# Optimization experiments

Measured on AMD Instinct MI355X. Metric: run time of the kernel, lower is better.

## Reference

```python
import jax, jax.numpy as jnp
import numpy as np


def setup_inputs() -> dict:
    key = jax.random.key(0)
    k1, k2 = jax.random.split(key, 2)
    x = jax.random.normal(k1, (16, 64, 256, 256), dtype=jnp.float32)
    w_off = jax.random.normal(k2, (2, 64), dtype=jnp.float32) * 0.05  # 1x1 conv kernel [out=2, in=ch]
    b_off = jnp.zeros((2,), dtype=jnp.float32)
    return {"x": x, "w_off": w_off, "b_off": b_off}


def _bilinear_grid_sample(x, gx, gy):
    """grid_sample(x, grid, align_corners=False, padding_mode='zeros').
    x: [B,C,H,W]; gx,gy: [B,H,W] normalized coords in [-1,1] (+offset)."""
    B, C, H, W = x.shape
    # unnormalize (align_corners=False): pix = ((g+1)*size - 1)/2
    px = ((gx + 1.0) * W - 1.0) * 0.5
    py = ((gy + 1.0) * H - 1.0) * 0.5
    x0f = jnp.floor(px)
    y0f = jnp.floor(py)
    wx1 = px - x0f  # frac weights
    wy1 = py - y0f
    x0 = x0f.astype(jnp.int32)
    y0 = y0f.astype(jnp.int32)

    def corner(xi, yi):
        valid = (xi >= 0) & (xi < W) & (yi >= 0) & (yi < H)
        xc = jnp.clip(xi, 0, W - 1)
        yc = jnp.clip(yi, 0, H - 1)
        # per-batch gather: img[:, yb, xb] -> [C,H,W]
        v = jax.vmap(lambda img, yb, xb: img[:, yb, xb])(x, yc, xc)  # [B,C,H,W]
        return v * valid[:, None, :, :].astype(x.dtype)

    v00 = corner(x0, y0)
    v01 = corner(x0 + 1, y0)
    v10 = corner(x0, y0 + 1)
    v11 = corner(x0 + 1, y0 + 1)
    wx1e = wx1[:, None, :, :]
    wy1e = wy1[:, None, :, :]
    return (v00 * (1.0 - wx1e) * (1.0 - wy1e)
            + v01 * wx1e * (1.0 - wy1e)
            + v10 * (1.0 - wx1e) * wy1e
            + v11 * wx1e * wy1e)


def reference(x, w_off, b_off):
    B, C, H, W = x.shape
    # 1x1 conv (ch -> 2) + tanh, scaled by 0.5
    offset = jnp.tanh(jnp.einsum('bchw,oc->bohw', x, w_off)
                      + b_off[None, :, None, None]) * 0.5  # [B,2,H,W]
    yy = jnp.linspace(-1.0, 1.0, H, dtype=x.dtype)
    xx = jnp.linspace(-1.0, 1.0, W, dtype=x.dtype)
    gy_base, gx_base = jnp.meshgrid(yy, xx, indexing='ij')  # [H,W]
    # grid = stack([xx, yy], -1) + offset.permute(0,2,3,1): channel0 -> x, channel1 -> y
    gx = gx_base[None] + offset[:, 0]
    gy = gy_base[None] + offset[:, 1]
    return _bilinear_grid_sample(x, gx, gy)
```

## Files before the change

### kernel.cpp

```cpp
#include <hip/hip_runtime.h>

#define BB 16
#define CC 64
#define HH 256
#define WW 256
#define HW (HH * WW)

#define XT_BYTES 134217728ULL
#define NEED_WS  (XT_BYTES + 8388608ULL)

typedef float    fx4 __attribute__((ext_vector_type(4)));
typedef unsigned ux4 __attribute__((ext_vector_type(4)));

__device__ __forceinline__ unsigned f2bf(float f) {
    unsigned u = __float_as_uint(f);
    u += 0x7FFFu + ((u >> 16) & 1u);
    return u >> 16;
}
__device__ __forceinline__ float bflo(unsigned w) { return __uint_as_float(w << 16); }
__device__ __forceinline__ float bfhi(unsigned w) { return __uint_as_float(w & 0xFFFF0000u); }

__global__ __launch_bounds__(256) void k_prep(
    const float* __restrict__ x, const float* __restrict__ w_off, const float* __restrict__ b_off,
    unsigned* __restrict__ xt, float2* __restrict__ pq)
{
    __shared__ unsigned s_pack[CC / 2][WW + 1];
    __shared__ float sw0[CC], sw1[CC];
    const int t = threadIdx.x;
    if (t < CC)          sw0[t]      = w_off[t];
    else if (t < 2 * CC) sw1[t - CC] = w_off[t];
    __syncthreads();
    const int row = blockIdx.x & (HH - 1);
    const int b   = blockIdx.x >> 8;
    const float* __restrict__ xb = x + (size_t)b * CC * HW + row * WW + t;
    float a0 = 0.f, a1 = 0.f, vprev = 0.f;
#pragma unroll 16
    for (int c = 0; c < CC; ++c) {
        const float v = xb[(size_t)c * HW];
        a0 = fmaf(v, sw0[c], a0);
        a1 = fmaf(v, sw1[c], a1);
        if (c & 1) s_pack[c >> 1][t] = f2bf(vprev) | (f2bf(v) << 16);
        vprev = v;
    }
    const float offx = tanhf(a0 + b_off[0]) * 0.5f;
    const float offy = tanhf(a1 + b_off[1]) * 0.5f;
    const float gx = -1.0f + (float)t   * (2.0f / (WW - 1)) + offx;
    const float gy = -1.0f + (float)row * (2.0f / (HH - 1)) + offy;
    pq[(size_t)b * HW + row * WW + t] =
        make_float2(((gx + 1.0f) * (float)WW - 1.0f) * 0.5f, ((gy + 1.0f) * (float)HH - 1.0f) * 0.5f);
    __syncthreads();
    const int j  = t & 7;
    const int pb = t >> 3;
    unsigned* __restrict__ xto = xt + ((size_t)b * HW + (size_t)row * WW) * 32;
#pragma unroll
    for (int g = 0; g < 8; ++g) {
        const int p = g * 32 + pb;
        ux4 v;
        v.x = s_pack[4 * j + 0][p];
        v.y = s_pack[4 * j + 1][p];
        v.z = s_pack[4 * j + 2][p];
        v.w = s_pack[4 * j + 3][p];
        __builtin_nontemporal_store(v, reinterpret_cast<ux4*>(xto + (size_t)p * 32 + j * 4));
    }
}

__global__ __launch_bounds__(256) void k_sample4(
    const unsigned* __restrict__ xt, const float2* __restrict__ pq, float* __restrict__ out)
{
    const int raw = blockIdx.x;
    const int lb  = (raw & 7) * 1024 + (raw >> 3);
    const int half = lb & 1;
    const int row  = (lb >> 1) & (HH - 1);
    const int b    = lb >> 9;

    __shared__ float so[2][CC][65];

    const int t  = threadIdx.x;
    const int l8 = t & 7;
    const int ps = t >> 3;
    const int px0 = half * 128;

    const unsigned* __restrict__ xb = xt + (size_t)b * HW * 32;
    const float2* __restrict__ pqr = pq + (size_t)b * HW + row * WW + px0;

    const float2 prA0 = pqr[ps];
    const float2 prB0 = pqr[32 + ps];
    const float2 prA1 = pqr[64 + ps];
    const float2 prB1 = pqr[96 + ps];

#define COORDS(prc, W00, W01, W10, W11, I00, I01, I10, I11)                         \
    {                                                                               \
        const float x0f = floorf(prc.x), y0f = floorf(prc.y);                       \
        const float wx1 = prc.x - x0f,  wy1 = prc.y - y0f;                          \
        const float wx0 = 1.f - wx1,   wy0 = 1.f - wy1;                             \
        const int x0 = (int)x0f, y0 = (int)y0f, x1 = x0 + 1, y1 = y0 + 1;           \
        const bool vx0 = (unsigned)x0 < WW, vx1 = (unsigned)x1 < WW;                \
        const bool vy0 = (unsigned)y0 < HH, vy1 = (unsigned)y1 < HH;                \
        const int cx0 = min(max(x0, 0), WW - 1), cx1 = min(max(x1, 0), WW - 1);     \
        const int cy0 = min(max(y0, 0), HH - 1), cy1 = min(max(y1, 0), HH - 1);     \
        W00 = (vx0 && vy0) ? wx0 * wy0 : 0.f;                                       \
        W01 = (vx1 && vy0) ? wx1 * wy0 : 0.f;                                       \
        W10 = (vx0 && vy1) ? wx0 * wy1 : 0.f;                                       \
        W11 = (vx1 && vy1) ? wx1 * wy1 : 0.f;                                       \
        I00 = (unsigned)(cy0 * WW + cx0) * 32u + l8 * 4u;                           \
        I01 = (unsigned)(cy0 * WW + cx1) * 32u + l8 * 4u;                           \
        I10 = (unsigned)(cy1 * WW + cx0) * 32u + l8 * 4u;                           \
        I11 = (unsigned)(cy1 * WW + cx1) * 32u + l8 * 4u;                           \
    }

    float wA00, wA01, wA10, wA11, wB00, wB01, wB10, wB11;
    float uA00, uA01, uA10, uA11, uB00, uB01, uB10, uB11;
    unsigned iA00, iA01, iA10, iA11, iB00, iB01, iB10, iB11;
    unsigned jA00, jA01, jA10, jA11, jB00, jB01, jB10, jB11;
    COORDS(prA0, wA00, wA01, wA10, wA11, iA00, iA01, iA10, iA11)
    COORDS(prB0, wB00, wB01, wB10, wB11, iB00, iB01, iB10, iB11)
    COORDS(prA1, uA00, uA01, uA10, uA11, jA00, jA01, jA10, jA11)
    COORDS(prB1, uB00, uB01, uB10, uB11, jB00, jB01, jB10, jB11)

    const uint4 vA00 = *reinterpret_cast<const uint4*>(xb + iA00);
    const uint4 vA01 = *reinterpret_cast<const uint4*>(xb + iA01);
    const uint4 vA10 = *reinterpret_cast<const uint4*>(xb + iA10);
    const uint4 vA11 = *reinterpret_cast<const uint4*>(xb + iA11);
    const uint4 vB00 = *reinterpret_cast<const uint4*>(xb + iB00);
    const uint4 vB01 = *reinterpret_cast<const uint4*>(xb + iB01);
    const uint4 vB10 = *reinterpret_cast<const uint4*>(xb + iB10);
    const uint4 vB11 = *reinterpret_cast<const uint4*>(xb + iB11);
    const uint4 yA00 = *reinterpret_cast<const uint4*>(xb + jA00);
    const uint4 yA01 = *reinterpret_cast<const uint4*>(xb + jA01);
    const uint4 yA10 = *reinterpret_cast<const uint4*>(xb + jA10);
    const uint4 yA11 = *reinterpret_cast<const uint4*>(xb + jA11);
    const uint4 yB00 = *reinterpret_cast<const uint4*>(xb + jB00);
    const uint4 yB01 = *reinterpret_cast<const uint4*>(xb + jB01);
    const uint4 yB10 = *reinterpret_cast<const uint4*>(xb + jB10);
    const uint4 yB11 = *reinterpret_cast<const uint4*>(xb + jB11);

    const int c8 = l8 * 8;

#define BLEND_STORE(BUF, V00, V01, V10, V11, W00, W01, W10, W11, PXL)               \
    {                                                                               \
        float f0 = W00 * bflo(V00.x); float f1 = W00 * bfhi(V00.x);                 \
        float f2 = W00 * bflo(V00.y); float f3 = W00 * bfhi(V00.y);                 \
        float f4 = W00 * bflo(V00.z); float f5 = W00 * bfhi(V00.z);                 \
        float f6 = W00 * bflo(V00.w); float f7 = W00 * bfhi(V00.w);                 \
        f0 = fmaf(W01, bflo(V01.x), f0); f1 = fmaf(W01, bfhi(V01.x), f1);           \
        f2 = fmaf(W01, bflo(V01.y), f2); f3 = fmaf(W01, bfhi(V01.y), f3);           \
        f4 = fmaf(W01, bflo(V01.z), f4); f5 = fmaf(W01, bfhi(V01.z), f5);           \
        f6 = fmaf(W01, bflo(V01.w), f6); f7 = fmaf(W01, bfhi(V01.w), f7);           \
        f0 = fmaf(W10, bflo(V10.x), f0); f1 = fmaf(W10, bfhi(V10.x), f1);           \
        f2 = fmaf(W10, bflo(V10.y), f2); f3 = fmaf(W10, bfhi(V10.y), f3);           \
        f4 = fmaf(W10, bflo(V10.z), f4); f5 = fmaf(W10, bfhi(V10.z), f5);           \
        f6 = fmaf(W10, bflo(V10.w), f6); f7 = fmaf(W10, bfhi(V10.w), f7);           \
        f0 = fmaf(W11, bflo(V11.x), f0); f1 = fmaf(W11, bfhi(V11.x), f1);           \
        f2 = fmaf(W11, bflo(V11.y), f2); f3 = fmaf(W11, bfhi(V11.y), f3);           \
        f4 = fmaf(W11, bflo(V11.z), f4); f5 = fmaf(W11, bfhi(V11.z), f5);           \
        f6 = fmaf(W11, bflo(V11.w), f6); f7 = fmaf(W11, bfhi(V11.w), f7);           \
        so[BUF][c8 + 0][PXL] = f0; so[BUF][c8 + 1][PXL] = f1;                       \
        so[BUF][c8 + 2][PXL] = f2; so[BUF][c8 + 3][PXL] = f3;                       \
        so[BUF][c8 + 4][PXL] = f4; so[BUF][c8 + 5][PXL] = f5;                       \
        so[BUF][c8 + 6][PXL] = f6; so[BUF][c8 + 7][PXL] = f7;                       \
    }

#define WRITEOUT(BUF, QOFF)                                                         \
    {                                                                               \
        const int p  = t & 15;                                                      \
        const int cg = (t >> 4) & 3;                                                \
        const int wv = t >> 6;                                                      \
        float* __restrict__ ob = out + (size_t)b * CC * HW + row * WW + px0 + QOFF; \
        _Pragma("unroll")                                                           \
        for (int it = 0; it < 4; ++it) {                                            \
            const int c = wv * 16 + it * 4 + cg;                                    \
            fx4 r;                                                                  \
            r.x = so[BUF][c][4 * p + 0];                                            \
            r.y = so[BUF][c][4 * p + 1];                                            \
            r.z = so[BUF][c][4 * p + 2];                                            \
            r.w = so[BUF][c][4 * p + 3];                                            \
            __builtin_nontemporal_store(r, reinterpret_cast<fx4*>(ob + (size_t)c * HW + 4 * p)); \
        }                                                                           \
    }

    BLEND_STORE(0, vA00, vA01, vA10, vA11, wA00, wA01, wA10, wA11, ps)
    BLEND_STORE(0, vB00, vB01, vB10, vB11, wB00, wB01, wB10, wB11, (32 + ps))
    __syncthreads();
    WRITEOUT(0, 0)
    BLEND_STORE(1, yA00, yA01, yA10, yA11, uA00, uA01, uA10, uA11, ps)
    BLEND_STORE(1, yB00, yB01, yB10, yB11, uB00, uB01, uB10, uB11, (32 + ps))
    __syncthreads();
    WRITEOUT(1, 64)
}

__global__ __launch_bounds__(256) void k_offsets(
    const float* __restrict__ x, const float* __restrict__ w_off, const float* __restrict__ b_off,
    float2* __restrict__ pq)
{
    __shared__ float s_w0[CC];
    __shared__ float s_w1[CC];
    if (threadIdx.x < CC)          s_w0[threadIdx.x]      = w_off[threadIdx.x];
    else if (threadIdx.x < 2 * CC) s_w1[threadIdx.x - CC] = w_off[threadIdx.x];
    __syncthreads();
    const int t    = blockIdx.x * blockDim.x + threadIdx.x;
    const int pix0 = t * 4;
    const int w = pix0 & (WW - 1);
    const int h = (pix0 >> 8) & (HH - 1);
    const int b = pix0 >> 16;
    const float* __restrict__ xb = x + (size_t)b * CC * HW + h * WW + w;
    float a0[4] = {0.f, 0.f, 0.f, 0.f};
    float a1[4] = {0.f, 0.f, 0.f, 0.f};
#pragma unroll 8
    for (int c = 0; c < CC; ++c) {
        const float4 v = *reinterpret_cast<const float4*>(xb + (size_t)c * HW);
        const float w0 = s_w0[c], w1 = s_w1[c];
        a0[0] = fmaf(v.x, w0, a0[0]); a1[0] = fmaf(v.x, w1, a1[0]);
        a0[1] = fmaf(v.y, w0, a0[1]); a1[1] = fmaf(v.y, w1, a1[1]);
        a0[2] = fmaf(v.z, w0, a0[2]); a1[2] = fmaf(v.z, w1, a1[2]);
        a0[3] = fmaf(v.w, w0, a0[3]); a1[3] = fmaf(v.w, w1, a1[3]);
    }
    const float b0 = b_off[0], b1 = b_off[1];
#pragma unroll
    for (int j = 0; j < 4; ++j) {
        const float offx = tanhf(a0[j] + b0) * 0.5f;
        const float offy = tanhf(a1[j] + b1) * 0.5f;
        const float gx = -1.0f + (float)(w + j) * (2.0f / (WW - 1)) + offx;
        const float gy = -1.0f + (float)h       * (2.0f / (HH - 1)) + offy;
        pq[pix0 + j] = make_float2(((gx + 1.0f) * (float)WW - 1.0f) * 0.5f,
                                   ((gy + 1.0f) * (float)HH - 1.0f) * 0.5f);
    }
}

__global__ __launch_bounds__(256, 4) void k_sample(
    const float* __restrict__ x, const float2* __restrict__ pq, float* __restrict__ out)
{
    const int bid = blockIdx.x;
    const int c = bid & (CC - 1);
    const int b = bid >> 6;
    const float* __restrict__ xp = x   + ((size_t)b * CC + c) * HW;
    float* __restrict__       op = out + ((size_t)b * CC + c) * HW;
    const float2* __restrict__ pqb = pq + (size_t)b * HW;
    const int w = threadIdx.x;
    for (int k0 = 0; k0 < HH; k0 += 4) {
        int   i00[4], i01[4], i10[4], i11[4];
        float w00[4], w01[4], w10[4], w11[4];
#pragma unroll
        for (int j = 0; j < 4; ++j) {
            const float2 p = pqb[(k0 + j) * WW + w];
            const float x0f = floorf(p.x);
            const float y0f = floorf(p.y);
            const float wx1 = p.x - x0f;
            const float wy1 = p.y - y0f;
            const float wx0 = 1.0f - wx1;
            const float wy0 = 1.0f - wy1;
            const int x0 = (int)x0f, y0 = (int)y0f;
            const int x1 = x0 + 1,   y1 = y0 + 1;
            const bool vx0 = (unsigned)x0 < WW;
            const bool vx1 = (unsigned)x1 < WW;
            const bool vy0 = (unsigned)y0 < HH;
            const bool vy1 = (unsigned)y1 < HH;
            const int cx0 = min(max(x0, 0), WW - 1);
            const int cx1 = min(max(x1, 0), WW - 1);
            const int cy0 = min(max(y0, 0), HH - 1);
            const int cy1 = min(max(y1, 0), HH - 1);
            w00[j] = (vx0 && vy0) ? wx0 * wy0 : 0.f;
            w01[j] = (vx1 && vy0) ? wx1 * wy0 : 0.f;
            w10[j] = (vx0 && vy1) ? wx0 * wy1 : 0.f;
            w11[j] = (vx1 && vy1) ? wx1 * wy1 : 0.f;
            i00[j] = cy0 * WW + cx0;
            i01[j] = cy0 * WW + cx1;
            i10[j] = cy1 * WW + cx0;
            i11[j] = cy1 * WW + cx1;
        }
        float v00[4], v01[4], v10[4], v11[4];
#pragma unroll
        for (int j = 0; j < 4; ++j) v00[j] = xp[i00[j]];
#pragma unroll
        for (int j = 0; j < 4; ++j) v01[j] = xp[i01[j]];
#pragma unroll
        for (int j = 0; j < 4; ++j) v10[j] = xp[i10[j]];
#pragma unroll
        for (int j = 0; j < 4; ++j) v11[j] = xp[i11[j]];
#pragma unroll
        for (int j = 0; j < 4; ++j) {
            float v = w00[j] * v00[j];
            v = fmaf(w01[j], v01[j], v);
            v = fmaf(w10[j], v10[j], v);
            v = fmaf(w11[j], v11[j], v);
            __builtin_nontemporal_store(v, &op[(k0 + j) * WW + w]);
        }
    }
}

extern "C" void kernel_launch(void* const* d_in, const int* in_sizes, int n_in,
                              void* d_out, int out_size, void* d_ws, size_t ws_size,
                              hipStream_t stream) {
    const float* x     = (const float*)d_in[0];
    const float* w_off = (const float*)d_in[1];
    const float* b_off = (const float*)d_in[2];
    float* out = (float*)d_out;

    if (ws_size >= NEED_WS) {
        unsigned* xt = (unsigned*)d_ws;
        float2*   pq = (float2*)((char*)d_ws + XT_BYTES);
        k_prep<<<BB * HH, 256, 0, stream>>>(x, w_off, b_off, xt, pq);
        k_sample4<<<BB * HH * 2, 256, 0, stream>>>(xt, pq, out);
    } else {
        float2* pq = (float2*)d_ws;
        const int grid1 = (BB * HW / 4) / 256;
        k_offsets<<<grid1, 256, 0, stream>>>(x, w_off, b_off, pq);
        k_sample<<<BB * CC, 256, 0, stream>>>(x, pq, out);
    }
}
```

Baseline: 189.1 us.

## Software-pipeline prep and sampling across batch groups with mixed-role kernels

Splits the batch into groups of four and launches mixed kernels whose blocks either transpose/pack the next group or sample the previous group, interleaved at a 1:2 ratio. The aim is to overlap the read-heavy prep phase with the gather/write-heavy sampling phase so both HBM directions and compute stay busy, and to shrink the bf16 working set touched at once so it stays more cache-resident. In exchange it adds launches, a shared-memory union sized to the larger role (possibly lowering occupancy), and block-role divergence.

```diff
diff --git a/kernel.cpp b/kernel.cpp
--- a/kernel.cpp
+++ b/kernel.cpp
@@ -9,6 +9,10 @@
 #define XT_BYTES 134217728ULL
 #define NEED_WS  (XT_BYTES + 8388608ULL)
 
+#define NBG   4
+#define PBLK  (NBG * HH)
+#define SBLK  (NBG * HH * 2)
+
 typedef float    fx4 __attribute__((ext_vector_type(4)));
 typedef unsigned ux4 __attribute__((ext_vector_type(4)));
 
@@ -20,73 +24,43 @@
 __device__ __forceinline__ float bflo(unsigned w) { return __uint_as_float(w << 16); }
 __device__ __forceinline__ float bfhi(unsigned w) { return __uint_as_float(w & 0xFFFF0000u); }
 
-__global__ __launch_bounds__(256) void k_prep(
-    const float* __restrict__ x, const float* __restrict__ w_off, const float* __restrict__ b_off,
-    unsigned* __restrict__ xt, float2* __restrict__ pq)
-{
-    __shared__ unsigned s_pack[CC / 2][WW + 1];
-    __shared__ float sw0[CC], sw1[CC];
-    const int t = threadIdx.x;
-    if (t < CC)          sw0[t]      = w_off[t];
-    else if (t < 2 * CC) sw1[t - CC] = w_off[t];
-    __syncthreads();
-    const int row = blockIdx.x & (HH - 1);
-    const int b   = blockIdx.x >> 8;
-    const float* __restrict__ xb = x + (size_t)b * CC * HW + row * WW + t;
-    float a0 = 0.f, a1 = 0.f, vprev = 0.f;
-#pragma unroll 16
-    for (int c = 0; c < CC; ++c) {
-        const float v = xb[(size_t)c * HW];
-        a0 = fmaf(v, sw0[c], a0);
-        a1 = fmaf(v, sw1[c], a1);
-        if (c & 1) s_pack[c >> 1][t] = f2bf(vprev) | (f2bf(v) << 16);
-        vprev = v;
-    }
-    const float offx = tanhf(a0 + b_off[0]) * 0.5f;
-    const float offy = tanhf(a1 + b_off[1]) * 0.5f;
-    const float gx = -1.0f + (float)t   * (2.0f / (WW - 1)) + offx;
-    const float gy = -1.0f + (float)row * (2.0f / (HH - 1)) + offy;
-    pq[(size_t)b * HW + row * WW + t] =
-        make_float2(((gx + 1.0f) * (float)WW - 1.0f) * 0.5f, ((gy + 1.0f) * (float)HH - 1.0f) * 0.5f);
-    __syncthreads();
-    const int j  = t & 7;
-    const int pb = t >> 3;
-    unsigned* __restrict__ xto = xt + ((size_t)b * HW + (size_t)row * WW) * 32;
-#pragma unroll
-    for (int g = 0; g < 8; ++g) {
-        const int p = g * 32 + pb;
-        ux4 v;
-        v.x = s_pack[4 * j + 0][p];
-        v.y = s_pack[4 * j + 1][p];
-        v.z = s_pack[4 * j + 2][p];
-        v.w = s_pack[4 * j + 3][p];
-        __builtin_nontemporal_store(v, reinterpret_cast<ux4*>(xto + (size_t)p * 32 + j * 4));
-    }
-}
-
-__global__ __launch_bounds__(256) void k_sample4(
-    const unsigned* __restrict__ xt, const float2* __restrict__ pq, float* __restrict__ out)
-{
-    const int raw = blockIdx.x;
-    const int lb  = (raw & 7) * 1024 + (raw >> 3);
-    const int half = lb & 1;
-    const int row  = (lb >> 1) & (HH - 1);
-    const int b    = lb >> 9;
-
-    __shared__ float so[2][CC][65];
-
-    const int t  = threadIdx.x;
-    const int l8 = t & 7;
-    const int ps = t >> 3;
-    const int px0 = half * 128;
-
-    const unsigned* __restrict__ xb = xt + (size_t)b * HW * 32;
-    const float2* __restrict__ pqr = pq + (size_t)b * HW + row * WW + px0;
-
-    const float2 prA0 = pqr[ps];
-    const float2 prB0 = pqr[32 + ps];
-    const float2 prA1 = pqr[64 + ps];
-    const float2 prB1 = pqr[96 + ps];
+#define PREP_BODY(B_, ROW_, PACK_, W0_, W1_)                                        \
+    {                                                                               \
+        if (t < CC)          W0_[t]      = w_off[t];                                \
+        else if (t < 2*CC)   W1_[t - CC] = w_off[t];                                \
+        __syncthreads();                                                            \
+        const float* __restrict__ xb = x + (size_t)(B_) * CC * HW + (ROW_) * WW + t;\
+        float a0 = 0.f, a1 = 0.f, vprev = 0.f;                                      \
+        _Pragma("unroll 16")                                                        \
+        for (int c = 0; c < CC; ++c) {                                              \
+            const float v = xb[(size_t)c * HW];                                     \
+            a0 = fmaf(v, W0_[c], a0);                                               \
+            a1 = fmaf(v, W1_[c], a1);                                               \
+            if (c & 1) PACK_[c >> 1][t] = f2bf(vprev) | (f2bf(v) << 16);            \
+            vprev = v;                                                              \
+        }                                                                           \
+        const float offx = tanhf(a0 + b_off[0]) * 0.5f;                             \
+        const float offy = tanhf(a1 + b_off[1]) * 0.5f;                             \
+        const float gx = -1.0f + (float)t      * (2.0f / (WW - 1)) + offx;          \
+        const float gy = -1.0f + (float)(ROW_) * (2.0f / (HH - 1)) + offy;          \
+        pq[(size_t)(B_) * HW + (ROW_) * WW + t] =                                   \
+            make_float2(((gx + 1.0f) * (float)WW - 1.0f) * 0.5f,                    \
+                        ((gy + 1.0f) * (float)HH - 1.0f) * 0.5f);                   \
+        __syncthreads();                                                            \
+        const int j  = t & 7;                                                       \
+        const int pb = t >> 3;                                                      \
+        unsigned* __restrict__ xto = xt + ((size_t)(B_) * HW + (size_t)(ROW_) * WW) * 32; \
+        _Pragma("unroll")                                                           \
+        for (int g = 0; g < 8; ++g) {                                               \
+            const int p = g * 32 + pb;                                              \
+            ux4 v;                                                                  \
+            v.x = PACK_[4 * j + 0][p];                                              \
+            v.y = PACK_[4 * j + 1][p];                                              \
+            v.z = PACK_[4 * j + 2][p];                                              \
+            v.w = PACK_[4 * j + 3][p];                                              \
+            __builtin_nontemporal_store(v, reinterpret_cast<ux4*>(xto + (size_t)p * 32 + j * 4)); \
+        }                                                                           \
+    }
 
 #define COORDS(prc, W00, W01, W10, W11, I00, I01, I10, I11)                         \
     {                                                                               \
@@ -108,35 +82,7 @@
         I11 = (unsigned)(cy1 * WW + cx1) * 32u + l8 * 4u;                           \
     }
 
-    float wA00, wA01, wA10, wA11, wB00, wB01, wB10, wB11;
-    float uA00, uA01, uA10, uA11, uB00, uB01, uB10, uB11;
-    unsigned iA00, iA01, iA10, iA11, iB00, iB01, iB10, iB11;
-    unsigned jA00, jA01, jA10, jA11, jB00, jB01, jB10, jB11;
-    COORDS(prA0, wA00, wA01, wA10, wA11, iA00, iA01, iA10, iA11)
-    COORDS(prB0, wB00, wB01, wB10, wB11, iB00, iB01, iB10, iB11)
-    COORDS(prA1, uA00, uA01, uA10, uA11, jA00, jA01, jA10, jA11)
-    COORDS(prB1, uB00, uB01, uB10, uB11, jB00, jB01, jB10, jB11)
-
-    const uint4 vA00 = *reinterpret_cast<const uint4*>(xb + iA00);
-    const uint4 vA01 = *reinterpret_cast<const uint4*>(xb + iA01);
-    const uint4 vA10 = *reinterpret_cast<const uint4*>(xb + iA10);
-    const uint4 vA11 = *reinterpret_cast<const uint4*>(xb + iA11);
-    const uint4 vB00 = *reinterpret_cast<const uint4*>(xb + iB00);
-    const uint4 vB01 = *reinterpret_cast<const uint4*>(xb + iB01);
-    const uint4 vB10 = *reinterpret_cast<const uint4*>(xb + iB10);
-    const uint4 vB11 = *reinterpret_cast<const uint4*>(xb + iB11);
-    const uint4 yA00 = *reinterpret_cast<const uint4*>(xb + jA00);
-    const uint4 yA01 = *reinterpret_cast<const uint4*>(xb + jA01);
-    const uint4 yA10 = *reinterpret_cast<const uint4*>(xb + jA10);
-    const uint4 yA11 = *reinterpret_cast<const uint4*>(xb + jA11);
-    const uint4 yB00 = *reinterpret_cast<const uint4*>(xb + jB00);
-    const uint4 yB01 = *reinterpret_cast<const uint4*>(xb + jB01);
-    const uint4 yB10 = *reinterpret_cast<const uint4*>(xb + jB10);
-    const uint4 yB11 = *reinterpret_cast<const uint4*>(xb + jB11);
-
-    const int c8 = l8 * 8;
-
-#define BLEND_STORE(BUF, V00, V01, V10, V11, W00, W01, W10, W11, PXL)               \
+#define BLEND_STORE(SO_, BUF, V00, V01, V10, V11, W00, W01, W10, W11, PXL)          \
     {                                                                               \
         float f0 = W00 * bflo(V00.x); float f1 = W00 * bfhi(V00.x);                 \
         float f2 = W00 * bflo(V00.y); float f3 = W00 * bfhi(V00.y);                 \
@@ -154,38 +100,127 @@
         f2 = fmaf(W11, bflo(V11.y), f2); f3 = fmaf(W11, bfhi(V11.y), f3);           \
         f4 = fmaf(W11, bflo(V11.z), f4); f5 = fmaf(W11, bfhi(V11.z), f5);           \
         f6 = fmaf(W11, bflo(V11.w), f6); f7 = fmaf(W11, bfhi(V11.w), f7);           \
-        so[BUF][c8 + 0][PXL] = f0; so[BUF][c8 + 1][PXL] = f1;                       \
-        so[BUF][c8 + 2][PXL] = f2; so[BUF][c8 + 3][PXL] = f3;                       \
-        so[BUF][c8 + 4][PXL] = f4; so[BUF][c8 + 5][PXL] = f5;                       \
-        so[BUF][c8 + 6][PXL] = f6; so[BUF][c8 + 7][PXL] = f7;                       \
-    }
-
-#define WRITEOUT(BUF, QOFF)                                                         \
+        SO_[BUF][c8 + 0][PXL] = f0; SO_[BUF][c8 + 1][PXL] = f1;                     \
+        SO_[BUF][c8 + 2][PXL] = f2; SO_[BUF][c8 + 3][PXL] = f3;                     \
+        SO_[BUF][c8 + 4][PXL] = f4; SO_[BUF][c8 + 5][PXL] = f5;                     \
+        SO_[BUF][c8 + 6][PXL] = f6; SO_[BUF][c8 + 7][PXL] = f7;                     \
+    }
+
+#define WRITEOUT(SO_, BUF, B_, ROW_, PX0_, QOFF)                                    \
     {                                                                               \
         const int p  = t & 15;                                                      \
         const int cg = (t >> 4) & 3;                                                \
         const int wv = t >> 6;                                                      \
-        float* __restrict__ ob = out + (size_t)b * CC * HW + row * WW + px0 + QOFF; \
+        float* __restrict__ ob = out + (size_t)(B_) * CC * HW + (ROW_) * WW + (PX0_) + QOFF; \
         _Pragma("unroll")                                                           \
         for (int it = 0; it < 4; ++it) {                                            \
             const int c = wv * 16 + it * 4 + cg;                                    \
             fx4 r;                                                                  \
-            r.x = so[BUF][c][4 * p + 0];                                            \
-            r.y = so[BUF][c][4 * p + 1];                                            \
-            r.z = so[BUF][c][4 * p + 2];                                            \
-            r.w = so[BUF][c][4 * p + 3];                                            \
+            r.x = SO_[BUF][c][4 * p + 0];                                           \
+            r.y = SO_[BUF][c][4 * p + 1];                                           \
+            r.z = SO_[BUF][c][4 * p + 2];                                           \
+            r.w = SO_[BUF][c][4 * p + 3];                                           \
             __builtin_nontemporal_store(r, reinterpret_cast<fx4*>(ob + (size_t)c * HW + 4 * p)); \
         }                                                                           \
     }
 
-    BLEND_STORE(0, vA00, vA01, vA10, vA11, wA00, wA01, wA10, wA11, ps)
-    BLEND_STORE(0, vB00, vB01, vB10, vB11, wB00, wB01, wB10, wB11, (32 + ps))
-    __syncthreads();
-    WRITEOUT(0, 0)
-    BLEND_STORE(1, yA00, yA01, yA10, yA11, uA00, uA01, uA10, uA11, ps)
-    BLEND_STORE(1, yB00, yB01, yB10, yB11, uB00, uB01, uB10, uB11, (32 + ps))
-    __syncthreads();
-    WRITEOUT(1, 64)
+#define SAMPLE_BODY(B_, ROW_, HALF_, SO_)                                           \
+    {                                                                               \
+        const int l8 = t & 7;                                                       \
+        const int ps = t >> 3;                                                      \
+        const int px0 = (HALF_) * 128;                                              \
+        const unsigned* __restrict__ xb = xt + (size_t)(B_) * HW * 32;              \
+        const float2* __restrict__ pqr = pq + (size_t)(B_) * HW + (ROW_) * WW + px0;\
+        const float2 prA0 = pqr[ps];                                                \
+        const float2 prB0 = pqr[32 + ps];                                           \
+        const float2 prA1 = pqr[64 + ps];                                           \
+        const float2 prB1 = pqr[96 + ps];                                           \
+        float wA00, wA01, wA10, wA11, wB00, wB01, wB10, wB11;                       \
+        float uA00, uA01, uA10, uA11, uB00, uB01, uB10, uB11;                       \
+        unsigned iA00, iA01, iA10, iA11, iB00, iB01, iB10, iB11;                    \
+        unsigned jA00, jA01, jA10, jA11, jB00, jB01, jB10, jB11;                    \
+        COORDS(prA0, wA00, wA01, wA10, wA11, iA00, iA01, iA10, iA11)                \
+        COORDS(prB0, wB00, wB01, wB10, wB11, iB00, iB01, iB10, iB11)                \
+        COORDS(prA1, uA00, uA01, uA10, uA11, jA00, jA01, jA10, jA11)                \
+        COORDS(prB1, uB00, uB01, uB10, uB11, jB00, jB01, jB10, jB11)                \
+        const uint4 vA00 = *reinterpret_cast<const uint4*>(xb + iA00);              \
+        const uint4 vA01 = *reinterpret_cast<const uint4*>(xb + iA01);              \
+        const uint4 vA10 = *reinterpret_cast<const uint4*>(xb + iA10);              \
+        const uint4 vA11 = *reinterpret_cast<const uint4*>(xb + iA11);              \
+        const uint4 vB00 = *reinterpret_cast<const uint4*>(xb + iB00);              \
+        const uint4 vB01 = *reinterpret_cast<const uint4*>(xb + iB01);              \
+        const uint4 vB10 = *reinterpret_cast<const uint4*>(xb + iB10);              \
+        const uint4 vB11 = *reinterpret_cast<const uint4*>(xb + iB11);              \
+        const uint4 yA00 = *reinterpret_cast<const uint4*>(xb + jA00);              \
+        const uint4 yA01 = *reinterpret_cast<const uint4*>(xb + jA01);              \
+        const uint4 yA10 = *reinterpret_cast<const uint4*>(xb + jA10);              \
+        const uint4 yA11 = *reinterpret_cast<const uint4*>(xb + jA11);              \
+        const uint4 yB00 = *reinterpret_cast<const uint4*>(xb + jB00);              \
+        const uint4 yB01 = *reinterpret_cast<const uint4*>(xb + jB01);              \
+        const uint4 yB10 = *reinterpret_cast<const uint4*>(xb + jB10);              \
+        const uint4 yB11 = *reinterpret_cast<const uint4*>(xb + jB11);              \
+        const int c8 = l8 * 8;                                                      \
+        BLEND_STORE(SO_, 0, vA00, vA01, vA10, vA11, wA00, wA01, wA10, wA11, ps)     \
+        BLEND_STORE(SO_, 0, vB00, vB01, vB10, vB11, wB00, wB01, wB10, wB11, (32 + ps)) \
+        __syncthreads();                                                            \
+        WRITEOUT(SO_, 0, B_, ROW_, px0, 0)                                          \
+        BLEND_STORE(SO_, 1, yA00, yA01, yA10, yA11, uA00, uA01, uA10, uA11, ps)     \
+        BLEND_STORE(SO_, 1, yB00, yB01, yB10, yB11, uB00, uB01, uB10, uB11, (32 + ps)) \
+        __syncthreads();                                                            \
+        WRITEOUT(SO_, 1, B_, ROW_, px0, 64)                                         \
+    }
+
+__global__ __launch_bounds__(256) void k_prep(
+    const float* __restrict__ x, const float* __restrict__ w_off, const float* __restrict__ b_off,
+    unsigned* __restrict__ xt, float2* __restrict__ pq, int pbase)
+{
+    __shared__ unsigned s_pack[CC / 2][WW + 1];
+    __shared__ float sw0[CC], sw1[CC];
+    const int t   = threadIdx.x;
+    const int bid = blockIdx.x;
+    const int b   = pbase + (bid >> 8);
+    const int row = bid & 255;
+    PREP_BODY(b, row, s_pack, sw0, sw1)
+}
+
+__global__ __launch_bounds__(256) void k_sample4(
+    const unsigned* __restrict__ xt, const float2* __restrict__ pq, float* __restrict__ out,
+    int sbase)
+{
+    __shared__ float so[2][CC][65];
+    const int t   = threadIdx.x;
+    const int raw = blockIdx.x;
+    const int lb  = (raw & 7) * (SBLK / 8) + (raw >> 3);
+    const int half = lb & 1;
+    const int row  = (lb >> 1) & (HH - 1);
+    const int b    = sbase + (lb >> 9);
+    SAMPLE_BODY(b, row, half, so)
+}
+
+union MixSh {
+    struct { unsigned pack[CC / 2][WW + 1]; float w0[CC], w1[CC]; } p;
+    float so[2][CC][65];
+};
+__global__ __launch_bounds__(256) void k_mix(
+    const float* __restrict__ x, const float* __restrict__ w_off, const float* __restrict__ b_off,
+    unsigned* __restrict__ xt, float2* __restrict__ pq, float* __restrict__ out,
+    int pbase, int sbase)
+{
+    __shared__ MixSh sh;
+    const int t   = threadIdx.x;
+    const int bid = blockIdx.x;
+    if (bid % 3 == 0) {
+        const int pidx = bid / 3;
+        const int b    = pbase + (pidx >> 8);
+        const int row  = pidx & 255;
+        PREP_BODY(b, row, sh.p.pack, sh.p.w0, sh.p.w1)
+    } else {
+        const int sidx = (bid / 3) * 2 + (bid % 3) - 1;
+        const int half = sidx & 1;
+        const int row  = (sidx >> 1) & (HH - 1);
+        const int b    = sbase + (sidx >> 9);
+        SAMPLE_BODY(b, row, half, sh.so)
+    }
 }
 
 __global__ __launch_bounds__(256) void k_offsets(
@@ -298,8 +333,11 @@
     if (ws_size >= NEED_WS) {
         unsigned* xt = (unsigned*)d_ws;
         float2*   pq = (float2*)((char*)d_ws + XT_BYTES);
-        k_prep<<<BB * HH, 256, 0, stream>>>(x, w_off, b_off, xt, pq);
-        k_sample4<<<BB * HH * 2, 256, 0, stream>>>(xt, pq, out);
+        k_prep   <<<PBLK,        256, 0, stream>>>(x, w_off, b_off, xt, pq, 0);
+        k_mix    <<<PBLK + SBLK, 256, 0, stream>>>(x, w_off, b_off, xt, pq, out,  4,  0);
+        k_mix    <<<PBLK + SBLK, 256, 0, stream>>>(x, w_off, b_off, xt, pq, out,  8,  4);
+        k_mix    <<<PBLK + SBLK, 256, 0, stream>>>(x, w_off, b_off, xt, pq, out, 12,  8);
+        k_sample4<<<SBLK,        256, 0, stream>>>(xt, pq, out, 12);
     } else {
         float2* pq = (float2*)d_ws;
         const int grid1 = (BB * HW / 4) / 256;
```

Measured after the change: 181.1 us. -4.2%, faster.
